# Kernel tuning notes

Hardware: AMD Instinct MI355X
Metric: run time of the kernel (lower is better)

## Reference

```python
import jax, jax.numpy as jnp
import numpy as np
import math

H = 16          # num_attention_heads
DH = 64         # attention_head_size
HID = 1024      # hidden_size


def _rotate_half(x):
    # stack([-x[...,1::2], x[...,::2]], -1).reshape_as(x)
    return jnp.stack([-x[..., 1::2], x[..., ::2]], axis=-1).reshape(x.shape)


def _apply_rope(sinusoidal_pos, q, k):
    sin, cos = jnp.split(sinusoidal_pos, 2, axis=-1)            # [1,1,S,DH/2] each
    sin_pos = jnp.stack([sin, sin], axis=-1).reshape(sinusoidal_pos.shape)
    cos_pos = jnp.stack([cos, cos], axis=-1).reshape(sinusoidal_pos.shape)
    q = q * cos_pos + _rotate_half(q) * sin_pos
    k = k * cos_pos + _rotate_half(k) * sin_pos
    return q, k


def _split_heads(x):
    B, S, _ = x.shape
    return x.reshape(B, S, H, DH).transpose(0, 2, 1, 3)         # [B,H,S,DH]


def setup_inputs() -> dict:
    key = jax.random.key(0)
    ks = jax.random.split(key, 5)
    B, S = 4, 2048
    x = jax.random.normal(ks[0], (B, S, HID), dtype=jnp.float32)
    attention_mask = jnp.zeros((B, 1, 1, S), dtype=jnp.float32)
    sinusoidal_pos = jax.random.normal(ks[1], (1, 1, S, DH), dtype=jnp.float32)
    scale = 1.0 / math.sqrt(HID)
    Wq = jax.random.normal(ks[2], (HID, HID), dtype=jnp.float32) * scale
    Wk = jax.random.normal(ks[3], (HID, HID), dtype=jnp.float32) * scale
    Wv = jax.random.normal(ks[4], (HID, HID), dtype=jnp.float32) * scale
    bq = jnp.zeros((HID,), dtype=jnp.float32)
    bk = jnp.zeros((HID,), dtype=jnp.float32)
    bv = jnp.zeros((HID,), dtype=jnp.float32)
    return {"x": x, "attention_mask": attention_mask, "sinusoidal_pos": sinusoidal_pos,
            "Wq": Wq, "bq": bq, "Wk": Wk, "bk": bk, "Wv": Wv, "bv": bv}


def reference(x, attention_mask, sinusoidal_pos, Wq, bq, Wk, bk, Wv, bv):
    # QKV projections (torch Linear: x @ W.T + b)
    q = _split_heads(x @ Wq.T + bq)                             # [B,H,S,DH]
    k = _split_heads(x @ Wk.T + bk)
    v = _split_heads(x @ Wv.T + bv)
    q, k = _apply_rope(sinusoidal_pos, q, k)
    scores = jnp.einsum('bhsd,bhtd->bhst', q, k) / math.sqrt(DH) + attention_mask
    probs = jax.nn.softmax(scores, axis=-1)                     # dropout p=0.0 -> identity
    ctx = jnp.einsum('bhst,bhtd->bhsd', probs, v)               # [B,H,S,DH]
    B, _, S, _ = ctx.shape
    return ctx.transpose(0, 2, 1, 3).reshape(B, S, HID)
```

## Files before the change

### kernel.cpp

```cpp
#include <hip/hip_runtime.h>
#include <stdint.h>

#define BATCH 4
#define SEQ   2048
#define NHEAD 16
#define DHEAD 64
#define HID   1024

typedef __bf16 bf16x8 __attribute__((ext_vector_type(8)));
typedef __bf16 bf16x4 __attribute__((ext_vector_type(4)));
typedef float  f32x4  __attribute__((ext_vector_type(4)));

__device__ __forceinline__ bf16x8 load8f(const float* p) {
  const f32x4 a = ((const f32x4*)p)[0];
  const f32x4 b = ((const f32x4*)p)[1];
  bf16x8 r;
#pragma unroll
  for (int i = 0; i < 4; ++i) r[i] = (__bf16)a[i];
#pragma unroll
  for (int i = 0; i < 4; ++i) r[4 + i] = (__bf16)b[i];
  return r;
}

__device__ __forceinline__ void gload_lds16(const __bf16* g, __bf16* l) {
  __builtin_amdgcn_global_load_lds(
      (const __attribute__((address_space(1))) uint32_t*)g,
      (__attribute__((address_space(3))) uint32_t*)l,
      16, 0, 0);
}

__global__ __launch_bounds__(256) void cvt_kernel(
    const float* __restrict__ src, __bf16* __restrict__ dst, int n8) {
  const int i = blockIdx.x * 256 + threadIdx.x;
  if (i < n8) *(bf16x8*)(dst + (size_t)i * 8) = load8f(src + (size_t)i * 8);
}

#define ASTRIDE 40
#define BK 32

__global__ __launch_bounds__(512) void qkv_bf16_kernel(
    const __bf16* __restrict__ xb, const __bf16* __restrict__ Wb,
    const float* __restrict__ bq, const float* __restrict__ bk,
    const float* __restrict__ bv, const float* __restrict__ sp,
    float* __restrict__ qout, __bf16* __restrict__ Kws, __bf16* __restrict__ Vws)
{
  const int widx = blockIdx.z;
  const __bf16* __restrict__ W    = Wb + (size_t)widx * HID * HID;
  const float*  __restrict__ bias = (widx == 0) ? bq : (widx == 1) ? bk : bv;

  const int m0   = blockIdx.y * 128;
  const int n0   = blockIdx.x * 128;
  const int tid  = threadIdx.x;
  const int lane = tid & 63;
  const int quad = lane >> 4;
  const int l16  = lane & 15;
  const int wave = tid >> 6;
  const int wr   = wave >> 1, wc = wave & 1;

  __shared__ __align__(16) __bf16 As[2][128 * BK];
  __shared__ __align__(16) __bf16 Bs[2][128 * BK];

  const int srow = wave * 16 + (lane >> 2);
  const int scol = (lane & 3) * 8;
  const __bf16* aglb = xb + (size_t)(m0 + srow) * HID + scol;
  const __bf16* bglb = W  + (size_t)(n0 + srow) * HID + scol;
  const int woff = wave * 512;

  f32x4 acc[2][4];
  const f32x4 z = {0.f, 0.f, 0.f, 0.f};
#pragma unroll
  for (int i = 0; i < 2; ++i)
#pragma unroll
    for (int j = 0; j < 4; ++j) acc[i][j] = z;

  gload_lds16(aglb, &As[0][woff]);
  gload_lds16(bglb, &Bs[0][woff]);
  __syncthreads();

#pragma unroll 1
  for (int k0 = 0; k0 < HID; k0 += 2 * BK) {
    {
      gload_lds16(aglb + (k0 + BK), &As[1][woff]);
      gload_lds16(bglb + (k0 + BK), &Bs[1][woff]);

      bf16x8 af[2], bfr[4];
#pragma unroll
      for (int mt = 0; mt < 2; ++mt)
        af[mt] = *(const bf16x8*)(&As[0][(wr * 32 + mt * 16 + l16) * BK + quad * 8]);
#pragma unroll
      for (int nt = 0; nt < 4; ++nt)
        bfr[nt] = *(const bf16x8*)(&Bs[0][(wc * 64 + nt * 16 + l16) * BK + quad * 8]);

      if (widx < 2) {
#pragma unroll
        for (int mt = 0; mt < 2; ++mt)
#pragma unroll
          for (int nt = 0; nt < 4; ++nt)
            acc[mt][nt] = __builtin_amdgcn_mfma_f32_16x16x32_bf16(af[mt], bfr[nt], acc[mt][nt], 0, 0, 0);
      } else {
#pragma unroll
        for (int mt = 0; mt < 2; ++mt)
#pragma unroll
          for (int nt = 0; nt < 4; ++nt)
            acc[mt][nt] = __builtin_amdgcn_mfma_f32_16x16x32_bf16(bfr[nt], af[mt], acc[mt][nt], 0, 0, 0);
      }
      __syncthreads();
    }
    {
      if (k0 + 2 * BK < HID) {
        gload_lds16(aglb + (k0 + 2 * BK), &As[0][woff]);
        gload_lds16(bglb + (k0 + 2 * BK), &Bs[0][woff]);
      }

      bf16x8 af[2], bfr[4];
#pragma unroll
      for (int mt = 0; mt < 2; ++mt)
        af[mt] = *(const bf16x8*)(&As[1][(wr * 32 + mt * 16 + l16) * BK + quad * 8]);
#pragma unroll
      for (int nt = 0; nt < 4; ++nt)
        bfr[nt] = *(const bf16x8*)(&Bs[1][(wc * 64 + nt * 16 + l16) * BK + quad * 8]);

      if (widx < 2) {
#pragma unroll
        for (int mt = 0; mt < 2; ++mt)
#pragma unroll
          for (int nt = 0; nt < 4; ++nt)
            acc[mt][nt] = __builtin_amdgcn_mfma_f32_16x16x32_bf16(af[mt], bfr[nt], acc[mt][nt], 0, 0, 0);
      } else {
#pragma unroll
        for (int mt = 0; mt < 2; ++mt)
#pragma unroll
          for (int nt = 0; nt < 4; ++nt)
            acc[mt][nt] = __builtin_amdgcn_mfma_f32_16x16x32_bf16(bfr[nt], af[mt], acc[mt][nt], 0, 0, 0);
      }
      __syncthreads();
    }
  }

  if (widx < 2) {
#pragma unroll
    for (int mt = 0; mt < 2; ++mt) {
#pragma unroll
      for (int nt = 0; nt < 4; ++nt) {
        const int n = n0 + wc * 64 + nt * 16 + l16;
        const int h = n >> 6, d = n & 63;
        const float bval = bias[n];
#pragma unroll
        for (int v = 0; v < 4; ++v) {
          const int m = m0 + wr * 32 + mt * 16 + quad * 4 + v;
          const int b = m >> 11, s = m & (SEQ - 1);
          float val = acc[mt][nt][v] + bval;
          float p  = __shfl_xor(val, 1);
          float sn = sp[s * 64 + (d >> 1)];
          float cs = sp[s * 64 + 32 + (d >> 1)];
          val = val * cs + ((d & 1) ? p : -p) * sn;
          if (widx == 0) {
            qout[((size_t)b * SEQ + s) * HID + n] = val;
          } else {
            Kws[(((size_t)b * NHEAD + h) * SEQ + s) * DHEAD + d] = (__bf16)val;
          }
        }
      }
    }
  } else {
#pragma unroll
    for (int mt = 0; mt < 2; ++mt) {
#pragma unroll
      for (int nt = 0; nt < 4; ++nt) {
        const int m = m0 + wr * 32 + mt * 16 + l16;
        const int b = m >> 11, s = m & (SEQ - 1);
#pragma unroll
        for (int v = 0; v < 4; ++v) {
          const int n = n0 + wc * 64 + nt * 16 + quad * 4 + v;
          const int h = n >> 6, d = n & 63;
          float val = acc[mt][nt][v] + bias[n];
          Vws[(((size_t)b * NHEAD + h) * DHEAD + d) * SEQ + s] = (__bf16)val;
        }
      }
    }
  }
}

__global__ __launch_bounds__(512) void qkv_f32_kernel(
    const float* __restrict__ x,
    const float* __restrict__ Wq, const float* __restrict__ bq,
    const float* __restrict__ Wk, const float* __restrict__ bk,
    const float* __restrict__ Wv, const float* __restrict__ bv,
    const float* __restrict__ sp,
    float* __restrict__ qout, __bf16* __restrict__ Kws, __bf16* __restrict__ Vws)
{
  const int widx = blockIdx.z;
  const float* __restrict__ W    = (widx == 0) ? Wq : (widx == 1) ? Wk : Wv;
  const float* __restrict__ bias = (widx == 0) ? bq : (widx == 1) ? bk : bv;

  const int m0   = blockIdx.y * 128;
  const int n0   = blockIdx.x * 128;
  const int tid  = threadIdx.x;
  const int lane = tid & 63;
  const int quad = lane >> 4;
  const int l16  = lane & 15;
  const int wave = tid >> 6;
  const int wr   = wave >> 1, wc = wave & 1;

  __shared__ __align__(16) __bf16 As[128 * ASTRIDE];
  __shared__ __align__(16) __bf16 Bs[128 * ASTRIDE];

  const int srow = tid >> 2;
  const int scb  = tid & 3;

  f32x4 acc[2][4];
  const f32x4 z = {0.f, 0.f, 0.f, 0.f};
#pragma unroll
  for (int i = 0; i < 2; ++i)
#pragma unroll
    for (int j = 0; j < 4; ++j) acc[i][j] = z;

  bf16x8 areg = load8f(x + (size_t)(m0 + srow) * HID + scb * 8);
  bf16x8 breg = load8f(W + (size_t)(n0 + srow) * HID + scb * 8);

  for (int k0 = 0; k0 < HID; k0 += 32) {
    __syncthreads();
    *(bf16x8*)(As + srow * ASTRIDE + scb * 8) = areg;
    *(bf16x8*)(Bs + srow * ASTRIDE + scb * 8) = breg;
    __syncthreads();

    if (k0 + 32 < HID) {
      areg = load8f(x + (size_t)(m0 + srow) * HID + (k0 + 32) + scb * 8);
      breg = load8f(W + (size_t)(n0 + srow) * HID + (k0 + 32) + scb * 8);
    }

    bf16x8 af[2], bfr[4];
#pragma unroll
    for (int mt = 0; mt < 2; ++mt)
      af[mt] = *(const bf16x8*)(As + (wr * 32 + mt * 16 + l16) * ASTRIDE + quad * 8);
#pragma unroll
    for (int nt = 0; nt < 4; ++nt)
      bfr[nt] = *(const bf16x8*)(Bs + (wc * 64 + nt * 16 + l16) * ASTRIDE + quad * 8);

    if (widx < 2) {
#pragma unroll
      for (int mt = 0; mt < 2; ++mt)
#pragma unroll
        for (int nt = 0; nt < 4; ++nt)
          acc[mt][nt] = __builtin_amdgcn_mfma_f32_16x16x32_bf16(af[mt], bfr[nt], acc[mt][nt], 0, 0, 0);
    } else {
#pragma unroll
      for (int mt = 0; mt < 2; ++mt)
#pragma unroll
        for (int nt = 0; nt < 4; ++nt)
          acc[mt][nt] = __builtin_amdgcn_mfma_f32_16x16x32_bf16(bfr[nt], af[mt], acc[mt][nt], 0, 0, 0);
    }
  }

  if (widx < 2) {
#pragma unroll
    for (int mt = 0; mt < 2; ++mt) {
#pragma unroll
      for (int nt = 0; nt < 4; ++nt) {
        const int n = n0 + wc * 64 + nt * 16 + l16;
        const int h = n >> 6, d = n & 63;
        const float bval = bias[n];
#pragma unroll
        for (int v = 0; v < 4; ++v) {
          const int m = m0 + wr * 32 + mt * 16 + quad * 4 + v;
          const int b = m >> 11, s = m & (SEQ - 1);
          float val = acc[mt][nt][v] + bval;
          float p  = __shfl_xor(val, 1);
          float sn = sp[s * 64 + (d >> 1)];
          float cs = sp[s * 64 + 32 + (d >> 1)];
          val = val * cs + ((d & 1) ? p : -p) * sn;
          if (widx == 0) {
            qout[((size_t)b * SEQ + s) * HID + n] = val;
          } else {
            Kws[(((size_t)b * NHEAD + h) * SEQ + s) * DHEAD + d] = (__bf16)val;
          }
        }
      }
    }
  } else {
#pragma unroll
    for (int mt = 0; mt < 2; ++mt) {
#pragma unroll
      for (int nt = 0; nt < 4; ++nt) {
        const int m = m0 + wr * 32 + mt * 16 + l16;
        const int b = m >> 11, s = m & (SEQ - 1);
#pragma unroll
        for (int v = 0; v < 4; ++v) {
          const int n = n0 + wc * 64 + nt * 16 + quad * 4 + v;
          const int h = n >> 6, d = n & 63;
          float val = acc[mt][nt][v] + bias[n];
          Vws[(((size_t)b * NHEAD + h) * DHEAD + d) * SEQ + s] = (__bf16)val;
        }
      }
    }
  }
}

#define KT 64
#define QSTR 72
#define LOG2E 1.44269504088896340736f
#define PSHIFT 12.0f

__global__ __launch_bounds__(512) void attn_kernel(
    float* __restrict__ qo,
    const __bf16* __restrict__ Kws, const __bf16* __restrict__ Vws,
    const float* __restrict__ mask)
{
  const int q0   = blockIdx.x * 128;
  const int bh   = blockIdx.y;
  const int b    = bh >> 4, h = bh & 15;
  const int tid  = threadIdx.x;
  const int lane = tid & 63;
  const int wave = tid >> 6;
  const int quad = lane >> 4;
  const int l16  = lane & 15;

  __shared__ __align__(16) __bf16 Ks[64 * QSTR];
  __shared__ __align__(16) __bf16 Vts[64 * QSTR];
  __shared__ __align__(16) __bf16 PS[128 * QSTR];

  const __bf16* kbase = Kws + (size_t)bh * SEQ * DHEAD;
  const __bf16* vbase = Vws + (size_t)bh * DHEAD * SEQ;

  bf16x8 qf[2];
#pragma unroll
  for (int ks = 0; ks < 2; ++ks)
    qf[ks] = load8f(qo + ((size_t)b * SEQ + q0 + wave * 16 + l16) * HID
                       + h * DHEAD + ks * 32 + quad * 8);

  f32x4 o_acc[4];
  const f32x4 z = {0.f, 0.f, 0.f, 0.f};
#pragma unroll
  for (int i = 0; i < 4; ++i) o_acc[i] = z;
  float l_part = 0.f;

  const int qrow = tid >> 3;
  const int qcb  = tid & 7;

  bf16x8 kreg = *(const bf16x8*)(kbase + (size_t)qrow * DHEAD + qcb * 8);
  bf16x8 vreg = *(const bf16x8*)(vbase + (size_t)qrow * SEQ + qcb * 8);

  const float SC2 = 0.125f * LOG2E;

  for (int t0 = 0; t0 < SEQ; t0 += KT) {
    *(bf16x8*)(Ks  + qrow * QSTR + qcb * 8) = kreg;
    *(bf16x8*)(Vts + qrow * QSTR + qcb * 8) = vreg;
    __syncthreads();

    if (t0 + KT < SEQ) {
      kreg = *(const bf16x8*)(kbase + (size_t)(t0 + KT + qrow) * DHEAD + qcb * 8);
      vreg = *(const bf16x8*)(vbase + (size_t)qrow * SEQ + (t0 + KT) + qcb * 8);
    }

    f32x4 sc[4];
#pragma unroll
    for (int nt = 0; nt < 4; ++nt) sc[nt] = z;

    __builtin_amdgcn_s_setprio(1);
#pragma unroll
    for (int ks = 0; ks < 2; ++ks) {
      bf16x8 kf[4];
#pragma unroll
      for (int nt = 0; nt < 4; ++nt)
        kf[nt] = *(const bf16x8*)(Ks + (nt * 16 + l16) * QSTR + ks * 32 + quad * 8);
#pragma unroll
      for (int nt = 0; nt < 4; ++nt)
        sc[nt] = __builtin_amdgcn_mfma_f32_16x16x32_bf16(kf[nt], qf[ks], sc[nt], 0, 0, 0);
    }
    __builtin_amdgcn_s_setprio(0);

    f32x4 mv4[4];
#pragma unroll
    for (int nt = 0; nt < 4; ++nt)
      mv4[nt] = *(const f32x4*)(mask + b * SEQ + t0 + nt * 16 + quad * 4);

    const int prow = wave * 16 + l16;
#pragma unroll
    for (int nt = 0; nt < 4; ++nt) {
      bf16x4 pk;
#pragma unroll
      for (int v = 0; v < 4; ++v) {
        const float p = __builtin_amdgcn_exp2f(sc[nt][v] * SC2 + mv4[nt][v] * LOG2E - PSHIFT);
        l_part += p;
        pk[v] = (__bf16)p;
      }
      *(bf16x4*)(PS + prow * QSTR + nt * 16 + quad * 4) = pk;
    }

    __builtin_amdgcn_s_setprio(1);
#pragma unroll
    for (int ks2 = 0; ks2 < 2; ++ks2) {
      bf16x8 pf = *(const bf16x8*)(PS + prow * QSTR + ks2 * 32 + quad * 8);
      bf16x8 vf[4];
#pragma unroll
      for (int db = 0; db < 4; ++db)
        vf[db] = *(const bf16x8*)(Vts + (db * 16 + l16) * QSTR + ks2 * 32 + quad * 8);
#pragma unroll
      for (int db = 0; db < 4; ++db)
        o_acc[db] = __builtin_amdgcn_mfma_f32_16x16x32_bf16(vf[db], pf, o_acc[db], 0, 0, 0);
    }
    __builtin_amdgcn_s_setprio(0);
    __syncthreads();
  }

  l_part += __shfl_xor(l_part, 16);
  l_part += __shfl_xor(l_part, 32);
  const float inv = 1.0f / l_part;

  const int s = q0 + wave * 16 + l16;
  float* op = qo + ((size_t)b * SEQ + s) * HID + h * DHEAD + quad * 4;
#pragma unroll
  for (int db = 0; db < 4; ++db) {
    f32x4 val = o_acc[db];
    val[0] *= inv; val[1] *= inv; val[2] *= inv; val[3] *= inv;
    *(f32x4*)(op + db * 16) = val;
  }
}

extern "C" void kernel_launch(void* const* d_in, const int* in_sizes, int n_in,
                              void* d_out, int out_size, void* d_ws, size_t ws_size,
                              hipStream_t stream) {
  const float* x    = (const float*)d_in[0];
  const float* mask = (const float*)d_in[1];
  const float* sp   = (const float*)d_in[2];
  const float* Wq   = (const float*)d_in[3];
  const float* bq   = (const float*)d_in[4];
  const float* Wk   = (const float*)d_in[5];
  const float* bk   = (const float*)d_in[6];
  const float* Wv   = (const float*)d_in[7];
  const float* bv   = (const float*)d_in[8];
  float* out = (float*)d_out;

  const size_t per = (size_t)BATCH * NHEAD * SEQ * DHEAD;
  const size_t wel = (size_t)3 * HID * HID;
  __bf16* Kws = (__bf16*)d_ws;
  __bf16* Vws = Kws + per;

  const size_t need = (2 * per + per + wel) * sizeof(__bf16);
  if (ws_size >= need) {
    __bf16* xb = Vws + per;
    __bf16* Wb = xb + per;
    cvt_kernel<<<(int)(per / 8 / 256), 256, 0, stream>>>(x, xb, (int)(per / 8));
    cvt_kernel<<<512, 256, 0, stream>>>(Wq, Wb, 131072);
    cvt_kernel<<<512, 256, 0, stream>>>(Wk, Wb + 1048576, 131072);
    cvt_kernel<<<512, 256, 0, stream>>>(Wv, Wb + 2097152, 131072);
    qkv_bf16_kernel<<<dim3(8, 64, 3), 512, 0, stream>>>(
        xb, Wb, bq, bk, bv, sp, out, Kws, Vws);
  } else {
    qkv_f32_kernel<<<dim3(8, 64, 3), 512, 0, stream>>>(
        x, Wq, bq, Wk, bk, Wv, bv, sp, out, Kws, Vws);
  }
  attn_kernel<<<dim3(16, 64), 512, 0, stream>>>(out, Kws, Vws, mask);
}
```

Measured before the change: 314.2 us.

## Double-buffer K/V tiles in attention and fuse fp32-to-bf16 conversion launches

The attention loop now keeps K and V tiles in two LDS buffers. The next tile is written into the alternate buffer while the current one is consumed, which removes one of the two __syncthreads per iteration. The four separate fp32-to-bf16 conversion launches for x, Wq, Wk and Wv are merged into one kernel that indexes into the right source, cutting launch overhead. This costs extra LDS per block, which may lower occupancy.

```diff
diff --git a/kernel.cpp b/kernel.cpp
--- a/kernel.cpp
+++ b/kernel.cpp
@@ -29,10 +29,28 @@
       16, 0, 0);
 }
 
-__global__ __launch_bounds__(256) void cvt_kernel(
-    const float* __restrict__ src, __bf16* __restrict__ dst, int n8) {
+#define XUNITS 1048576
+#define WUNITS 131072
+
+__global__ __launch_bounds__(256) void cvt_fused_kernel(
+    const float* __restrict__ x,
+    const float* __restrict__ Wq, const float* __restrict__ Wk,
+    const float* __restrict__ Wv,
+    __bf16* __restrict__ xb, __bf16* __restrict__ Wb) {
   const int i = blockIdx.x * 256 + threadIdx.x;
-  if (i < n8) *(bf16x8*)(dst + (size_t)i * 8) = load8f(src + (size_t)i * 8);
+  const float* s;
+  __bf16* d;
+  if (i < XUNITS) {
+    s = x + (size_t)i * 8;
+    d = xb + (size_t)i * 8;
+  } else {
+    const int j = i - XUNITS;
+    const int w = j >> 17;
+    const int o = j & (WUNITS - 1);
+    s = (w == 0 ? Wq : w == 1 ? Wk : Wv) + (size_t)o * 8;
+    d = Wb + ((size_t)w << 20) + (size_t)o * 8;
+  }
+  *(bf16x8*)d = load8f(s);
 }
 
 #define ASTRIDE 40
@@ -315,8 +333,8 @@
   const int quad = lane >> 4;
   const int l16  = lane & 15;
 
-  __shared__ __align__(16) __bf16 Ks[64 * QSTR];
-  __shared__ __align__(16) __bf16 Vts[64 * QSTR];
+  __shared__ __align__(16) __bf16 Ks[2][64 * QSTR];
+  __shared__ __align__(16) __bf16 Vts[2][64 * QSTR];
   __shared__ __align__(16) __bf16 PS[128 * QSTR];
 
   const __bf16* kbase = Kws + (size_t)bh * SEQ * DHEAD;
@@ -336,20 +354,30 @@
 
   const int qrow = tid >> 3;
   const int qcb  = tid & 7;
+  const int soff = qrow * QSTR + qcb * 8;
 
   bf16x8 kreg = *(const bf16x8*)(kbase + (size_t)qrow * DHEAD + qcb * 8);
   bf16x8 vreg = *(const bf16x8*)(vbase + (size_t)qrow * SEQ + qcb * 8);
+  *(bf16x8*)(&Ks[0][soff])  = kreg;
+  *(bf16x8*)(&Vts[0][soff]) = vreg;
+  kreg = *(const bf16x8*)(kbase + (size_t)(KT + qrow) * DHEAD + qcb * 8);
+  vreg = *(const bf16x8*)(vbase + (size_t)qrow * SEQ + KT + qcb * 8);
+  __syncthreads();
 
   const float SC2 = 0.125f * LOG2E;
+  int cur = 0;
 
   for (int t0 = 0; t0 < SEQ; t0 += KT) {
-    *(bf16x8*)(Ks  + qrow * QSTR + qcb * 8) = kreg;
-    *(bf16x8*)(Vts + qrow * QSTR + qcb * 8) = vreg;
-    __syncthreads();
+    const __bf16* kcur = &Ks[cur][0];
+    const __bf16* vcur = &Vts[cur][0];
 
     if (t0 + KT < SEQ) {
-      kreg = *(const bf16x8*)(kbase + (size_t)(t0 + KT + qrow) * DHEAD + qcb * 8);
-      vreg = *(const bf16x8*)(vbase + (size_t)qrow * SEQ + (t0 + KT) + qcb * 8);
+      *(bf16x8*)(&Ks[cur ^ 1][soff])  = kreg;
+      *(bf16x8*)(&Vts[cur ^ 1][soff]) = vreg;
+    }
+    if (t0 + 2 * KT < SEQ) {
+      kreg = *(const bf16x8*)(kbase + (size_t)(t0 + 2 * KT + qrow) * DHEAD + qcb * 8);
+      vreg = *(const bf16x8*)(vbase + (size_t)qrow * SEQ + (t0 + 2 * KT) + qcb * 8);
     }
 
     f32x4 sc[4];
@@ -362,7 +390,7 @@
       bf16x8 kf[4];
 #pragma unroll
       for (int nt = 0; nt < 4; ++nt)
-        kf[nt] = *(const bf16x8*)(Ks + (nt * 16 + l16) * QSTR + ks * 32 + quad * 8);
+        kf[nt] = *(const bf16x8*)(kcur + (nt * 16 + l16) * QSTR + ks * 32 + quad * 8);
 #pragma unroll
       for (int nt = 0; nt < 4; ++nt)
         sc[nt] = __builtin_amdgcn_mfma_f32_16x16x32_bf16(kf[nt], qf[ks], sc[nt], 0, 0, 0);
@@ -394,13 +422,15 @@
       bf16x8 vf[4];
 #pragma unroll
       for (int db = 0; db < 4; ++db)
-        vf[db] = *(const bf16x8*)(Vts + (db * 16 + l16) * QSTR + ks2 * 32 + quad * 8);
+        vf[db] = *(const bf16x8*)(vcur + (db * 16 + l16) * QSTR + ks2 * 32 + quad * 8);
 #pragma unroll
       for (int db = 0; db < 4; ++db)
         o_acc[db] = __builtin_amdgcn_mfma_f32_16x16x32_bf16(vf[db], pf, o_acc[db], 0, 0, 0);
     }
     __builtin_amdgcn_s_setprio(0);
+
     __syncthreads();
+    cur ^= 1;
   }
 
   l_part += __shfl_xor(l_part, 16);
@@ -440,10 +470,7 @@
   if (ws_size >= need) {
     __bf16* xb = Vws + per;
     __bf16* Wb = xb + per;
-    cvt_kernel<<<(int)(per / 8 / 256), 256, 0, stream>>>(x, xb, (int)(per / 8));
-    cvt_kernel<<<512, 256, 0, stream>>>(Wq, Wb, 131072);
-    cvt_kernel<<<512, 256, 0, stream>>>(Wk, Wb + 1048576, 131072);
-    cvt_kernel<<<512, 256, 0, stream>>>(Wv, Wb + 2097152, 131072);
+    cvt_fused_kernel<<<5632, 256, 0, stream>>>(x, Wq, Wk, Wv, xb, Wb);
     qkv_bf16_kernel<<<dim3(8, 64, 3), 512, 0, stream>>>(
         xb, Wb, bq, bk, bv, sp, out, Kws, Vws);
   } else {
```

New measurement: 308.0 us. 2.0% less time.
